# Performance work log

Measured on AMD Instinct MI355X. Metric: run time of the kernel, lower is better.

## Reference

```python
import jax, jax.numpy as jnp
import numpy as np

N = 25000   # nodes
E = 400000  # edges
F_IN = 128  # in_features
F_E = 16    # edge_features
C = 32      # channel_width
F_OUT = 1   # out_features
SLOPE = 0.01  # torch LeakyReLU default negative_slope


def leaky_relu(x):
    return jnp.where(x >= 0, x, SLOPE * x)


def setup_inputs() -> dict:
    key = jax.random.key(0)
    ks = jax.random.split(key, 12)
    x = jax.random.normal(ks[0], (N, F_IN), dtype=jnp.float32)
    edge_index = jax.random.randint(ks[1], (2, E), 0, N, dtype=jnp.int64)
    edge_attr = jax.random.normal(ks[2], (E, F_E), dtype=jnp.float32)
    # parameters (scaled like kaiming-ish fan-in init)
    W_in = jax.random.normal(ks[3], (F_IN, C), dtype=jnp.float32) / np.sqrt(F_IN)
    b_in = jnp.zeros((C,), dtype=jnp.float32)
    W_edge = jax.random.normal(ks[4], (F_E, C * C), dtype=jnp.float32) / np.sqrt(F_E)
    b_edge = jnp.zeros((C * C,), dtype=jnp.float32)
    W_root = jax.random.normal(ks[5], (C, C), dtype=jnp.float32) / np.sqrt(C)
    b_conv = jnp.zeros((C,), dtype=jnp.float32)
    W_out = jax.random.normal(ks[6], (C, F_OUT), dtype=jnp.float32) / np.sqrt(C)
    b_out = jnp.zeros((F_OUT,), dtype=jnp.float32)
    return {
        "x": x, "edge_index": edge_index, "edge_attr": edge_attr,
        "W_in": W_in, "b_in": b_in, "W_edge": W_edge, "b_edge": b_edge,
        "W_root": W_root, "b_conv": b_conv, "W_out": W_out, "b_out": b_out,
    }


def reference(x, edge_index, edge_attr, W_in, b_in, W_edge, b_edge,
              W_root, b_conv, W_out, b_out):
    # input projection (dropout = identity in eval mode)
    h = leaky_relu(x @ W_in + b_in)                       # [N, C]

    # NNConv layer (gnn_depth = 1):
    # per-edge weight matrix from edge_nn: Linear + LeakyReLU
    We = leaky_relu(edge_attr @ W_edge + b_edge)          # [E, C*C]
    We = We.reshape(E, C, C)                              # [E, C, C]
    src, dst = edge_index[0], edge_index[1]               # PyG: j=source, i=target
    # gather source node features, per-edge matvec, scatter-add to targets
    msg = jnp.einsum('ec,eco->eo', h[src], We)            # [E, C]
    aggr = jax.ops.segment_sum(msg, dst, num_segments=N)  # [N, C]
    h = aggr + h @ W_root + b_conv                        # root weight + bias
    h = leaky_relu(h)

    return h @ W_out + b_out                              # [N, F_OUT]
```

## Files before the change

### kernel.cpp

```cpp
#include <hip/hip_runtime.h>

#define NN 25000
#define EE 400000
#define FIN 128
#define FE 16
#define CH 32
#define SLOPE 0.01f
#define PROJ_BLOCKS 391
#define AUX_BLOCKS 32
#define WROW 24
#define WTP_SHORTS (1024 * WROW + 8)

typedef __attribute__((ext_vector_type(8))) short bf16x8;
typedef __attribute__((ext_vector_type(4))) float f32x4;

__device__ __forceinline__ float lrelu(float v) { return fmaxf(v, SLOPE * v); }

__device__ __forceinline__ f32x4 lrelu4(f32x4 v) {
    f32x4 s = v * SLOPE;
#if __has_builtin(__builtin_elementwise_max)
    return __builtin_elementwise_max(v, s);
#else
    f32x4 r;
    r[0] = fmaxf(v[0], s[0]); r[1] = fmaxf(v[1], s[1]);
    r[2] = fmaxf(v[2], s[2]); r[3] = fmaxf(v[3], s[3]);
    return r;
#endif
}

__device__ __forceinline__ short f2bf(float f) {
    union { float f; unsigned u; } v; v.f = f;
    unsigned r = (v.u + 0x7fffu + ((v.u >> 16) & 1u)) >> 16;
    return (short)r;
}

__global__ void __launch_bounds__(256)
k_pre(const float* __restrict__ x, const float* __restrict__ W_in,
      const float* __restrict__ b_in, const float* __restrict__ W_edge,
      const float* __restrict__ b_edge,
      float* __restrict__ h, float* __restrict__ aggr, short* __restrict__ WtP) {
    __shared__ short Wt1[CH * 136];
    int tid = threadIdx.x;

    if (blockIdx.x >= PROJ_BLOCKS) {
        int ab = blockIdx.x - PROJ_BLOCKS;
        if (ab < 4) {
            int co = ab * 256 + tid;
            short row[WROW] __attribute__((aligned(16)));
#pragma unroll
            for (int k = 0; k < 16; k++) row[k] = f2bf(W_edge[k * 1024 + co]);
            row[16] = f2bf(b_edge[co]);
#pragma unroll
            for (int k = 17; k < WROW; k++) row[k] = 0;
            uint4* dstp = (uint4*)(WtP + co * WROW);
            dstp[0] = ((uint4*)row)[0]; dstp[1] = ((uint4*)row)[1]; dstp[2] = ((uint4*)row)[2];
            if (ab == 0 && tid < 8) WtP[1024 * WROW + tid] = 0;
        } else {
            int t = (ab - 4) * 256 + tid;
            float4 z = make_float4(0.f, 0.f, 0.f, 0.f);
            for (int i = t; i < NN * CH / 4; i += (AUX_BLOCKS - 4) * 256)
                ((float4*)aggr)[i] = z;
        }
        return;
    }

#pragma unroll
    for (int i = 0; i < 16; i++) {
        int id = tid + 256 * i;
        int k = id >> 5, c = id & 31;
        Wt1[c * 136 + k] = f2bf(W_in[id]);
    }
    __syncthreads();

    int wave = tid >> 6, lane = tid & 63;
    int n16 = lane & 15, quad = lane >> 4;
    int node0 = blockIdx.x * 64 + wave * 16;

    f32x4 D[2];
#pragma unroll
    for (int ch = 0; ch < 2; ch++) {
        float bb = b_in[ch * 16 + n16];
        D[ch] = (f32x4){bb, bb, bb, bb};
    }
    int arow = node0 + n16; if (arow >= NN) arow = NN - 1;
#pragma unroll
    for (int kb = 0; kb < 4; kb++) {
        const float4* xp = (const float4*)(x + (size_t)arow * FIN + kb * 32 + quad * 8);
        float4 xa = xp[0], xb = xp[1];
        bf16x8 A = (bf16x8){f2bf(xa.x), f2bf(xa.y), f2bf(xa.z), f2bf(xa.w),
                            f2bf(xb.x), f2bf(xb.y), f2bf(xb.z), f2bf(xb.w)};
#pragma unroll
        for (int ch = 0; ch < 2; ch++) {
            bf16x8 B = *(const bf16x8*)&Wt1[(ch * 16 + n16) * 136 + kb * 32 + quad * 8];
            D[ch] = __builtin_amdgcn_mfma_f32_16x16x32_bf16(A, B, D[ch], 0, 0, 0);
        }
    }
#pragma unroll
    for (int ch = 0; ch < 2; ch++)
#pragma unroll
        for (int r = 0; r < 4; r++) {
            int nn = node0 + quad * 4 + r;
            if (nn < NN) h[(size_t)nn * CH + ch * 16 + n16] = lrelu(D[ch][r]);
        }
}

__global__ void __launch_bounds__(256, 2)
k_edge(const short* __restrict__ WtP,
       const float* __restrict__ ea,
       const int* __restrict__ src,
       const int* __restrict__ dst,
       const float* __restrict__ h,
       float* __restrict__ aggr) {
    __shared__ short WtL[WTP_SHORTS];
    __shared__ float hsT[CH * 132];

    int tid = threadIdx.x;
    int e0 = blockIdx.x * 128;

#pragma unroll
    for (int j = 0; j < 13; j++) {
        int idx = tid + 256 * j;
        if (idx < WTP_SHORTS / 8) ((uint4*)WtL)[idx] = ((const uint4*)WtP)[idx];
    }
    {
        int e = tid >> 1, half = tid & 1;
        int s = src[e0 + e];
        const float4* hp = (const float4*)(h + (size_t)s * CH + half * 16);
        float vv[16] __attribute__((aligned(16)));
        *(float4*)&vv[0] = hp[0]; *(float4*)&vv[4] = hp[1];
        *(float4*)&vv[8] = hp[2]; *(float4*)&vv[12] = hp[3];
#pragma unroll
        for (int j = 0; j < 16; j++) hsT[(half * 16 + j) * 132 + e] = vv[j];
    }
    __syncthreads();

    int wave = tid >> 6, lane = tid & 63;
    int n16 = lane & 15, quad = lane >> 4;
    int t0 = wave * 32, t1 = t0 + 16;

    bf16x8 A0 = (bf16x8){0,0,0,0,0,0,0,0}, A1 = A0;
    if (quad < 2) {
        const float4* p0 = (const float4*)(ea + (size_t)(e0 + t0 + n16) * FE + quad * 8);
        float4 a = p0[0], b = p0[1];
        A0 = (bf16x8){f2bf(a.x), f2bf(a.y), f2bf(a.z), f2bf(a.w),
                      f2bf(b.x), f2bf(b.y), f2bf(b.z), f2bf(b.w)};
        const float4* p1 = (const float4*)(ea + (size_t)(e0 + t1 + n16) * FE + quad * 8);
        a = p1[0]; b = p1[1];
        A1 = (bf16x8){f2bf(a.x), f2bf(a.y), f2bf(a.z), f2bf(a.w),
                      f2bf(b.x), f2bf(b.y), f2bf(b.z), f2bf(b.w)};
    } else if (quad == 2) {
        A0[0] = (short)0x3F80; A1[0] = (short)0x3F80;
    }

    f32x4 m0[2], m1[2];
    m0[0] = (f32x4){0,0,0,0}; m0[1] = m0[0]; m1[0] = m0[0]; m1[1] = m0[0];
    const f32x4 Z = (f32x4){0,0,0,0};

    const short* Bbase = WtL + n16 * WROW + quad * 8;
    const float* h0b = hsT + t0 + quad * 4;
    const float* h1b = hsT + t1 + quad * 4;

#pragma unroll
    for (int c4 = 0; c4 < 8; c4++) {
#pragma unroll
        for (int cc = 0; cc < 4; cc++) {
            int c = c4 * 4 + cc;
            f32x4 hc0 = *(const f32x4*)(h0b + c * 132);
            f32x4 hc1 = *(const f32x4*)(h1b + c * 132);
#pragma unroll
            for (int oh = 0; oh < 2; oh++) {
                int cb = c * 2 + oh;
                bf16x8 B = *(const bf16x8*)(Bbase + cb * (16 * WROW));
                f32x4 D0 = __builtin_amdgcn_mfma_f32_16x16x32_bf16(A0, B, Z, 0, 0, 0);
                f32x4 D1 = __builtin_amdgcn_mfma_f32_16x16x32_bf16(A1, B, Z, 0, 0, 0);
                m0[oh] += hc0 * lrelu4(D0);
                m1[oh] += hc1 * lrelu4(D1);
            }
        }
    }

#pragma unroll
    for (int r = 0; r < 4; r++) {
        int ed0 = dst[e0 + t0 + quad * 4 + r];
        int ed1 = dst[e0 + t1 + quad * 4 + r];
#pragma unroll
        for (int oh = 0; oh < 2; oh++) {
            unsafeAtomicAdd(&aggr[(size_t)ed0 * CH + oh * 16 + n16], m0[oh][r]);
            unsafeAtomicAdd(&aggr[(size_t)ed1 * CH + oh * 16 + n16], m1[oh][r]);
        }
    }
}

__global__ void __launch_bounds__(256)
k_node(const float* __restrict__ aggr,
       const float* __restrict__ h,
       const float* __restrict__ W_root,
       const float* __restrict__ b_conv,
       const float* __restrict__ W_out,
       const float* __restrict__ b_out,
       float* __restrict__ out) {
    __shared__ short WrB[CH * 40];
    __shared__ float WoS[CH];
    int tid = threadIdx.x;
    if (tid < 128) {
        int o = tid >> 2, c0 = (tid & 3) * 8;
        short tmp[8] __attribute__((aligned(16)));
#pragma unroll
        for (int j = 0; j < 8; j++) tmp[j] = f2bf(W_root[(c0 + j) * CH + o]);
        *(bf16x8*)&WrB[o * 40 + c0] = *(bf16x8*)tmp;
    } else if (tid < 160) {
        WoS[tid - 128] = W_out[tid - 128];
    }
    __syncthreads();

    int wave = tid >> 6, lane = tid & 63;
    int n16 = lane & 15, quad = lane >> 4;
    int node0 = blockIdx.x * 64 + wave * 16;

    int arow = node0 + n16; if (arow >= NN) arow = NN - 1;
    const float4* hp = (const float4*)(h + (size_t)arow * CH + quad * 8);
    float4 ha = hp[0], hb = hp[1];
    bf16x8 A = (bf16x8){f2bf(ha.x), f2bf(ha.y), f2bf(ha.z), f2bf(ha.w),
                        f2bf(hb.x), f2bf(hb.y), f2bf(hb.z), f2bf(hb.w)};
    float bc0 = b_conv[n16], bc1 = b_conv[16 + n16];
    f32x4 C0, C1;
#pragma unroll
    for (int r = 0; r < 4; r++) {
        int nr = node0 + quad * 4 + r; int cr = (nr < NN) ? nr : NN - 1;
        C0[r] = aggr[(size_t)cr * CH + n16] + bc0;
        C1[r] = aggr[(size_t)cr * CH + 16 + n16] + bc1;
    }
    bf16x8 B0 = *(const bf16x8*)&WrB[n16 * 40 + quad * 8];
    bf16x8 B1 = *(const bf16x8*)&WrB[(16 + n16) * 40 + quad * 8];
    f32x4 D0 = __builtin_amdgcn_mfma_f32_16x16x32_bf16(A, B0, C0, 0, 0, 0);
    f32x4 D1 = __builtin_amdgcn_mfma_f32_16x16x32_bf16(A, B1, C1, 0, 0, 0);

    float w0 = WoS[n16], w1 = WoS[16 + n16];
    f32x4 p;
#pragma unroll
    for (int r = 0; r < 4; r++)
        p[r] = lrelu(D0[r]) * w0 + lrelu(D1[r]) * w1;
#pragma unroll
    for (int mk = 1; mk < 16; mk <<= 1) {
#pragma unroll
        for (int r = 0; r < 4; r++) p[r] += __shfl_xor(p[r], mk, 64);
    }
    if (n16 == 0) {
        float bo = b_out[0];
#pragma unroll
        for (int r = 0; r < 4; r++) {
            int nr = node0 + quad * 4 + r;
            if (nr < NN) out[nr] = p[r] + bo;
        }
    }
}

extern "C" void kernel_launch(void* const* d_in, const int* in_sizes, int n_in,
                              void* d_out, int out_size, void* d_ws, size_t ws_size,
                              hipStream_t stream) {
    const float* x      = (const float*)d_in[0];
    const int*   ei     = (const int*)d_in[1];
    const float* ea     = (const float*)d_in[2];
    const float* W_in   = (const float*)d_in[3];
    const float* b_in   = (const float*)d_in[4];
    const float* W_edge = (const float*)d_in[5];
    const float* b_edge = (const float*)d_in[6];
    const float* W_root = (const float*)d_in[7];
    const float* b_conv = (const float*)d_in[8];
    const float* W_out  = (const float*)d_in[9];
    const float* b_out  = (const float*)d_in[10];
    float* out  = (float*)d_out;
    float* h    = (float*)d_ws;
    float* aggr = h + (size_t)NN * CH;
    short* WtP  = (short*)(aggr + (size_t)NN * CH);

    k_pre<<<PROJ_BLOCKS + AUX_BLOCKS, 256, 0, stream>>>(x, W_in, b_in, W_edge, b_edge,
                                                        h, aggr, WtP);
    k_edge<<<EE / 128, 256, 0, stream>>>(WtP, ea, ei, ei + EE, h, aggr);
    k_node<<<PROJ_BLOCKS, 256, 0, stream>>>(aggr, h, W_root, b_conv, W_out, b_out, out);
}
```

Baseline: 168.9 us.

## Double edges per block to amortize shared-memory weight staging

```diff
diff --git a/kernel.cpp b/kernel.cpp
--- a/kernel.cpp
+++ b/kernel.cpp
@@ -10,6 +10,8 @@
 #define AUX_BLOCKS 32
 #define WROW 24
 #define WTP_SHORTS (1024 * WROW + 8)
+#define EPB 256
+#define EDGE_BLOCKS ((EE + EPB - 1) / EPB)
 
 typedef __attribute__((ext_vector_type(8))) short bf16x8;
 typedef __attribute__((ext_vector_type(4))) float f32x4;
@@ -104,33 +106,35 @@
         }
 }
 
-__global__ void __launch_bounds__(256, 2)
+__global__ void __launch_bounds__(512, 4)
 k_edge(const short* __restrict__ WtP,
        const float* __restrict__ ea,
        const int* __restrict__ src,
        const int* __restrict__ dst,
        const float* __restrict__ h,
        float* __restrict__ aggr) {
-    __shared__ short WtL[WTP_SHORTS];
-    __shared__ float hsT[CH * 132];
+    __shared__ __align__(16) char smem[81920];
+    short* WtL = (short*)smem;
+    float* hsT = (float*)(smem + 49152);
 
     int tid = threadIdx.x;
-    int e0 = blockIdx.x * 128;
-
-#pragma unroll
-    for (int j = 0; j < 13; j++) {
-        int idx = tid + 256 * j;
-        if (idx < WTP_SHORTS / 8) ((uint4*)WtL)[idx] = ((const uint4*)WtP)[idx];
+    int e0 = blockIdx.x * EPB;
+
+#pragma unroll
+    for (int j = 0; j < 6; j++) {
+        int idx = tid + 512 * j;
+        ((uint4*)WtL)[idx] = ((const uint4*)WtP)[idx];
     }
     {
         int e = tid >> 1, half = tid & 1;
-        int s = src[e0 + e];
+        int ei = e0 + e; if (ei >= EE) ei = EE - 1;
+        int s = src[ei];
         const float4* hp = (const float4*)(h + (size_t)s * CH + half * 16);
         float vv[16] __attribute__((aligned(16)));
         *(float4*)&vv[0] = hp[0]; *(float4*)&vv[4] = hp[1];
         *(float4*)&vv[8] = hp[2]; *(float4*)&vv[12] = hp[3];
 #pragma unroll
-        for (int j = 0; j < 16; j++) hsT[(half * 16 + j) * 132 + e] = vv[j];
+        for (int j = 0; j < 16; j++) hsT[(half * 16 + j) * EPB + e] = vv[j];
     }
     __syncthreads();
 
@@ -140,11 +144,13 @@
 
     bf16x8 A0 = (bf16x8){0,0,0,0,0,0,0,0}, A1 = A0;
     if (quad < 2) {
-        const float4* p0 = (const float4*)(ea + (size_t)(e0 + t0 + n16) * FE + quad * 8);
+        int i0 = e0 + t0 + n16; if (i0 >= EE) i0 = EE - 1;
+        int i1 = e0 + t1 + n16; if (i1 >= EE) i1 = EE - 1;
+        const float4* p0 = (const float4*)(ea + (size_t)i0 * FE + quad * 8);
         float4 a = p0[0], b = p0[1];
         A0 = (bf16x8){f2bf(a.x), f2bf(a.y), f2bf(a.z), f2bf(a.w),
                       f2bf(b.x), f2bf(b.y), f2bf(b.z), f2bf(b.w)};
-        const float4* p1 = (const float4*)(ea + (size_t)(e0 + t1 + n16) * FE + quad * 8);
+        const float4* p1 = (const float4*)(ea + (size_t)i1 * FE + quad * 8);
         a = p1[0]; b = p1[1];
         A1 = (bf16x8){f2bf(a.x), f2bf(a.y), f2bf(a.z), f2bf(a.w),
                       f2bf(b.x), f2bf(b.y), f2bf(b.z), f2bf(b.w)};
@@ -156,7 +162,8 @@
     m0[0] = (f32x4){0,0,0,0}; m0[1] = m0[0]; m1[0] = m0[0]; m1[1] = m0[0];
     const f32x4 Z = (f32x4){0,0,0,0};
 
-    const short* Bbase = WtL + n16 * WROW + quad * 8;
+    int qoff = (quad == 3) ? 0 : quad * 8;
+    const short* Bbase = WtL + n16 * WROW + qoff;
     const float* h0b = hsT + t0 + quad * 4;
     const float* h1b = hsT + t1 + quad * 4;
 
@@ -165,8 +172,8 @@
 #pragma unroll
         for (int cc = 0; cc < 4; cc++) {
             int c = c4 * 4 + cc;
-            f32x4 hc0 = *(const f32x4*)(h0b + c * 132);
-            f32x4 hc1 = *(const f32x4*)(h1b + c * 132);
+            f32x4 hc0 = *(const f32x4*)(h0b + c * EPB);
+            f32x4 hc1 = *(const f32x4*)(h1b + c * EPB);
 #pragma unroll
             for (int oh = 0; oh < 2; oh++) {
                 int cb = c * 2 + oh;
@@ -181,12 +188,19 @@
 
 #pragma unroll
     for (int r = 0; r < 4; r++) {
-        int ed0 = dst[e0 + t0 + quad * 4 + r];
-        int ed1 = dst[e0 + t1 + quad * 4 + r];
-#pragma unroll
-        for (int oh = 0; oh < 2; oh++) {
-            unsafeAtomicAdd(&aggr[(size_t)ed0 * CH + oh * 16 + n16], m0[oh][r]);
-            unsafeAtomicAdd(&aggr[(size_t)ed1 * CH + oh * 16 + n16], m1[oh][r]);
+        int i0 = e0 + t0 + quad * 4 + r;
+        int i1 = e0 + t1 + quad * 4 + r;
+        if (i0 < EE) {
+            int ed0 = dst[i0];
+#pragma unroll
+            for (int oh = 0; oh < 2; oh++)
+                unsafeAtomicAdd(&aggr[(size_t)ed0 * CH + oh * 16 + n16], m0[oh][r]);
+        }
+        if (i1 < EE) {
+            int ed1 = dst[i1];
+#pragma unroll
+            for (int oh = 0; oh < 2; oh++)
+                unsafeAtomicAdd(&aggr[(size_t)ed1 * CH + oh * 16 + n16], m1[oh][r]);
         }
     }
 }
@@ -276,6 +290,6 @@
 
     k_pre<<<PROJ_BLOCKS + AUX_BLOCKS, 256, 0, stream>>>(x, W_in, b_in, W_edge, b_edge,
                                                         h, aggr, WtP);
-    k_edge<<<EE / 128, 256, 0, stream>>>(WtP, ea, ei, ei + EE, h, aggr);
+    k_edge<<<EDGE_BLOCKS, 512, 0, stream>>>(WtP, ea, ei, ei + EE, h, aggr);
     k_node<<<PROJ_BLOCKS, 256, 0, stream>>>(aggr, h, W_root, b_conv, W_out, b_out, out);
 }
```

After: 669.0 us. 296% more time.

## Make edge kernel persistent with double-buffered prefetch and rotated weight layout

Applied to the files above, without the earlier changes.

```diff
diff --git a/kernel.cpp b/kernel.cpp
--- a/kernel.cpp
+++ b/kernel.cpp
@@ -9,7 +9,9 @@
 #define PROJ_BLOCKS 391
 #define AUX_BLOCKS 32
 #define WROW 24
-#define WTP_SHORTS (1024 * WROW + 8)
+#define WTP_SHORTS (1024 * WROW)
+#define NTILES (EE / 128)
+#define PBLK 1024
 
 typedef __attribute__((ext_vector_type(8))) short bf16x8;
 typedef __attribute__((ext_vector_type(4))) float f32x4;
@@ -53,8 +55,12 @@
 #pragma unroll
             for (int k = 17; k < WROW; k++) row[k] = 0;
             uint4* dstp = (uint4*)(WtP + co * WROW);
-            dstp[0] = ((uint4*)row)[0]; dstp[1] = ((uint4*)row)[1]; dstp[2] = ((uint4*)row)[2];
-            if (ab == 0 && tid < 8) WtP[1024 * WROW + tid] = 0;
+            int p0 = co % 3;
+            int p1 = p0 + 1; if (p1 == 3) p1 = 0;
+            int p2 = p1 + 1; if (p2 == 3) p2 = 0;
+            dstp[p0] = ((uint4*)row)[0];
+            dstp[p1] = ((uint4*)row)[1];
+            dstp[p2] = ((uint4*)row)[2];
         } else {
             int t = (ab - 4) * 256 + tid;
             float4 z = make_float4(0.f, 0.f, 0.f, 0.f);
@@ -112,82 +118,125 @@
        const float* __restrict__ h,
        float* __restrict__ aggr) {
     __shared__ short WtL[WTP_SHORTS];
-    __shared__ float hsT[CH * 132];
+    __shared__ float hsT[2][CH * 128];
 
     int tid = threadIdx.x;
-    int e0 = blockIdx.x * 128;
-
-#pragma unroll
-    for (int j = 0; j < 13; j++) {
+
+#pragma unroll
+    for (int j = 0; j < 12; j++) {
         int idx = tid + 256 * j;
-        if (idx < WTP_SHORTS / 8) ((uint4*)WtL)[idx] = ((const uint4*)WtP)[idx];
-    }
-    {
-        int e = tid >> 1, half = tid & 1;
-        int s = src[e0 + e];
-        const float4* hp = (const float4*)(h + (size_t)s * CH + half * 16);
-        float vv[16] __attribute__((aligned(16)));
-        *(float4*)&vv[0] = hp[0]; *(float4*)&vv[4] = hp[1];
-        *(float4*)&vv[8] = hp[2]; *(float4*)&vv[12] = hp[3];
-#pragma unroll
-        for (int j = 0; j < 16; j++) hsT[(half * 16 + j) * 132 + e] = vv[j];
-    }
-    __syncthreads();
-
+        ((uint4*)WtL)[idx] = ((const uint4*)WtP)[idx];
+    }
+
+    int eH = tid >> 1, halfH = tid & 1;
     int wave = tid >> 6, lane = tid & 63;
     int n16 = lane & 15, quad = lane >> 4;
     int t0 = wave * 32, t1 = t0 + 16;
 
-    bf16x8 A0 = (bf16x8){0,0,0,0,0,0,0,0}, A1 = A0;
-    if (quad < 2) {
-        const float4* p0 = (const float4*)(ea + (size_t)(e0 + t0 + n16) * FE + quad * 8);
-        float4 a = p0[0], b = p0[1];
-        A0 = (bf16x8){f2bf(a.x), f2bf(a.y), f2bf(a.z), f2bf(a.w),
-                      f2bf(b.x), f2bf(b.y), f2bf(b.z), f2bf(b.w)};
-        const float4* p1 = (const float4*)(ea + (size_t)(e0 + t1 + n16) * FE + quad * 8);
-        a = p1[0]; b = p1[1];
-        A1 = (bf16x8){f2bf(a.x), f2bf(a.y), f2bf(a.z), f2bf(a.w),
-                      f2bf(b.x), f2bf(b.y), f2bf(b.z), f2bf(b.w)};
-    } else if (quad == 2) {
-        A0[0] = (short)0x3F80; A1[0] = (short)0x3F80;
-    }
-
-    f32x4 m0[2], m1[2];
-    m0[0] = (f32x4){0,0,0,0}; m0[1] = m0[0]; m1[0] = m0[0]; m1[1] = m0[0];
-    const f32x4 Z = (f32x4){0,0,0,0};
-
-    const short* Bbase = WtL + n16 * WROW + quad * 8;
-    const float* h0b = hsT + t0 + quad * 4;
-    const float* h1b = hsT + t1 + quad * 4;
-
-#pragma unroll
-    for (int c4 = 0; c4 < 8; c4++) {
-#pragma unroll
-        for (int cc = 0; cc < 4; cc++) {
-            int c = c4 * 4 + cc;
-            f32x4 hc0 = *(const f32x4*)(h0b + c * 132);
-            f32x4 hc1 = *(const f32x4*)(h1b + c * 132);
+    int s0 = (quad == 3) ? 0 : quad;
+    int rot = (s0 + n16) % 3;
+    const short* Bb[3];
+#pragma unroll
+    for (int j = 0; j < 3; j++) {
+        int p = rot + j; if (p >= 3) p -= 3;
+        Bb[j] = WtL + n16 * WROW + p * 8;
+    }
+
+    struct PrefT {
+        float hv[16];
+        float4 e0a, e0b, e1a, e1b;
+        int d[8];
+    };
+    PrefT Pa, Pb;
+
+    auto PREF = [&](int tile, PrefT& P) {
+        int base = tile * 128;
+        int s = src[base + eH];
+        const float4* hp = (const float4*)(h + (size_t)s * CH + halfH * 16);
+        float4 v0 = hp[0], v1 = hp[1], v2 = hp[2], v3 = hp[3];
+        *(float4*)&P.hv[0] = v0;  *(float4*)&P.hv[4] = v1;
+        *(float4*)&P.hv[8] = v2;  *(float4*)&P.hv[12] = v3;
+        if (quad < 2) {
+            const float4* p0 = (const float4*)(ea + (size_t)(base + t0 + n16) * FE + quad * 8);
+            P.e0a = p0[0]; P.e0b = p0[1];
+            const float4* p1 = (const float4*)(ea + (size_t)(base + t1 + n16) * FE + quad * 8);
+            P.e1a = p1[0]; P.e1b = p1[1];
+        }
+#pragma unroll
+        for (int r = 0; r < 4; r++) {
+            P.d[r]     = dst[base + t0 + quad * 4 + r];
+            P.d[4 + r] = dst[base + t1 + quad * 4 + r];
+        }
+    };
+
+    auto WRITE = [&](float* hbuf, PrefT& P) {
+        float* hd = hbuf + halfH * (16 * 128) + eH;
+#pragma unroll
+        for (int j = 0; j < 16; j++) hd[j * 128] = P.hv[j];
+    };
+
+    auto COMPUTE = [&](const float* hbuf, PrefT& P) {
+        bf16x8 A0 = (bf16x8){0,0,0,0,0,0,0,0}, A1 = A0;
+        if (quad < 2) {
+            A0 = (bf16x8){f2bf(P.e0a.x), f2bf(P.e0a.y), f2bf(P.e0a.z), f2bf(P.e0a.w),
+                          f2bf(P.e0b.x), f2bf(P.e0b.y), f2bf(P.e0b.z), f2bf(P.e0b.w)};
+            A1 = (bf16x8){f2bf(P.e1a.x), f2bf(P.e1a.y), f2bf(P.e1a.z), f2bf(P.e1a.w),
+                          f2bf(P.e1b.x), f2bf(P.e1b.y), f2bf(P.e1b.z), f2bf(P.e1b.w)};
+        } else if (quad == 2) {
+            A0[0] = (short)0x3F80; A1[0] = (short)0x3F80;
+        }
+
+        f32x4 m0[2], m1[2];
+        m0[0] = (f32x4){0,0,0,0}; m0[1] = m0[0]; m1[0] = m0[0]; m1[1] = m0[0];
+        const f32x4 Z = (f32x4){0,0,0,0};
+        const float* h0b = hbuf + t0 + quad * 4;
+        const float* h1b = hbuf + t1 + quad * 4;
+
+#pragma unroll
+        for (int c = 0; c < 32; c++) {
+            f32x4 hc0 = *(const f32x4*)(h0b + c * 128);
+            f32x4 hc1 = *(const f32x4*)(h1b + c * 128);
 #pragma unroll
             for (int oh = 0; oh < 2; oh++) {
                 int cb = c * 2 + oh;
-                bf16x8 B = *(const bf16x8*)(Bbase + cb * (16 * WROW));
+                bf16x8 B = *(const bf16x8*)(Bb[cb % 3] + cb * (16 * WROW));
                 f32x4 D0 = __builtin_amdgcn_mfma_f32_16x16x32_bf16(A0, B, Z, 0, 0, 0);
                 f32x4 D1 = __builtin_amdgcn_mfma_f32_16x16x32_bf16(A1, B, Z, 0, 0, 0);
                 m0[oh] += hc0 * lrelu4(D0);
                 m1[oh] += hc1 * lrelu4(D1);
             }
         }
-    }
-
-#pragma unroll
-    for (int r = 0; r < 4; r++) {
-        int ed0 = dst[e0 + t0 + quad * 4 + r];
-        int ed1 = dst[e0 + t1 + quad * 4 + r];
-#pragma unroll
-        for (int oh = 0; oh < 2; oh++) {
-            unsafeAtomicAdd(&aggr[(size_t)ed0 * CH + oh * 16 + n16], m0[oh][r]);
-            unsafeAtomicAdd(&aggr[(size_t)ed1 * CH + oh * 16 + n16], m1[oh][r]);
-        }
+
+#pragma unroll
+        for (int r = 0; r < 4; r++) {
+#pragma unroll
+            for (int oh = 0; oh < 2; oh++) {
+                unsafeAtomicAdd(&aggr[(size_t)P.d[r]     * CH + oh * 16 + n16], m0[oh][r]);
+                unsafeAtomicAdd(&aggr[(size_t)P.d[4 + r] * CH + oh * 16 + n16], m1[oh][r]);
+            }
+        }
+    };
+
+    int tile = blockIdx.x;
+    PREF(tile, Pa);
+    while (true) {
+        WRITE(&hsT[0][0], Pa);
+        __syncthreads();
+        int nt = tile + PBLK;
+        bool more = (nt < NTILES);
+        if (more) PREF(nt, Pb);
+        COMPUTE(&hsT[0][0], Pa);
+        if (!more) break;
+        tile = nt;
+
+        WRITE(&hsT[1][0], Pb);
+        __syncthreads();
+        nt = tile + PBLK;
+        more = (nt < NTILES);
+        if (more) PREF(nt, Pa);
+        COMPUTE(&hsT[1][0], Pb);
+        if (!more) break;
+        tile = nt;
     }
 }
 
@@ -276,6 +325,6 @@
 
     k_pre<<<PROJ_BLOCKS + AUX_BLOCKS, 256, 0, stream>>>(x, W_in, b_in, W_edge, b_edge,
                                                         h, aggr, WtP);
-    k_edge<<<EE / 128, 256, 0, stream>>>(WtP, ea, ei, ei + EE, h, aggr);
+    k_edge<<<PBLK, 256, 0, stream>>>(WtP, ea, ei, ei + EE, h, aggr);
     k_node<<<PROJ_BLOCKS, 256, 0, stream>>>(aggr, h, W_root, b_conv, W_out, b_out, out);
 }
```

Measured after the change: 163.6 us. -3.1%, faster.
